# Kernel optimization log

Hardware: AMD Instinct MI355X
Metric: run time of the kernel (lower is better)

Reference implementation:

```python
import jax, jax.numpy as jnp
import numpy as np

B, S, D = 2, 2048, 2048
H = 16
HD = D // H  # 128
ROPE_THETA = 10000.0
NEG_INF = -1e9


def _rope_tables(seqlen, head_dim):
    inv = 1.0 / (ROPE_THETA ** (np.arange(0, head_dim, 2, dtype=np.float32) / head_dim))
    t = np.arange(seqlen, dtype=np.float32)
    freqs = np.outer(t, inv)  # (S, HD/2)
    return jnp.asarray(np.cos(freqs)), jnp.asarray(np.sin(freqs))


def _apply_rope(x, cos, sin):
    # x: (B, S, H, HD); cos/sin: (S, HD/2) -> complex multiply on (even, odd) pairs
    x = x.reshape(*x.shape[:-1], HD // 2, 2)
    x0, x1 = x[..., 0], x[..., 1]
    c = cos[None, :, None, :]
    s = sin[None, :, None, :]
    o0 = x0 * c - x1 * s
    o1 = x0 * s + x1 * c
    return jnp.stack([o0, o1], axis=-1).reshape(*x.shape[:-2], HD)


def setup_inputs() -> dict:
    key = jax.random.key(0)
    ks = jax.random.split(key, 6)
    std = 1.0 / np.sqrt(D)
    x = jax.random.normal(ks[0], (B, S, D), dtype=jnp.float32)
    wq = jax.random.normal(ks[1], (D, D), dtype=jnp.float32) * std
    wk = jax.random.normal(ks[2], (D, D), dtype=jnp.float32) * std
    wv = jax.random.normal(ks[3], (D, D), dtype=jnp.float32) * std
    wo = jax.random.normal(ks[4], (D, D), dtype=jnp.float32) * std
    cos, sin = _rope_tables(S, HD)
    # additive causal mask
    mask = jnp.where(jnp.tril(jnp.ones((S, S), dtype=bool)), 0.0, NEG_INF).astype(jnp.float32)
    return {"x": x, "wq": wq, "wk": wk, "wv": wv, "wo": wo, "cos": cos, "sin": sin, "mask": mask, "start_p": 0}


def reference(x, wq, wk, wv, wo, cos, sin, mask, start_p):
    bsz, seqlen, _ = x.shape
    xq = (x @ wq.T).reshape(bsz, seqlen, H, HD)
    xk = (x @ wk.T).reshape(bsz, seqlen, H, HD)
    xv = (x @ wv.T).reshape(bsz, seqlen, H, HD)
    c = cos[start_p:start_p + seqlen]
    s = sin[start_p:start_p + seqlen]
    xq = _apply_rope(xq, c, s)
    xk = _apply_rope(xk, c, s)
    # (B, H, S, HD)
    q = xq.transpose(0, 2, 1, 3)
    k = xk.transpose(0, 2, 1, 3)
    v = xv.transpose(0, 2, 1, 3)
    scores = jnp.einsum("bhqd,bhkd->bhqk", q, k) / np.sqrt(HD).astype(np.float32)
    scores = scores + mask[None, None, :, :]
    probs = jax.nn.softmax(scores.astype(jnp.float32), axis=-1).astype(q.dtype)
    out = jnp.einsum("bhqk,bhkd->bhqd", probs, v)
    out = out.transpose(0, 2, 1, 3).reshape(bsz, seqlen, H * HD)
    return out @ wo.T
```

## Files before the change

kernel.cpp:

```cpp
#include <hip/hip_runtime.h>
#include <cstdint>
#include <cstddef>

typedef unsigned short u16;
typedef unsigned int u32;
typedef __attribute__((ext_vector_type(8))) short short8;
typedef __attribute__((ext_vector_type(2))) unsigned int u32x2;
typedef __attribute__((ext_vector_type(8))) __bf16 bf16x8;
typedef __attribute__((ext_vector_type(4))) float f32x4;

#define BB 2
#define SS 2048
#define DD 2048
#define HH 16
#define HD 128

__device__ __forceinline__ u16 f2bf(float x) {
  u32 u = __float_as_uint(x);
  u32 r = (u + 0x7FFFu + ((u >> 16) & 1u)) >> 16;
  return (u16)r;
}
__device__ __forceinline__ float bf2f(u16 h) {
  return __uint_as_float(((u32)h) << 16);
}
__device__ __forceinline__ float exp2_hw(float x) {
  return __builtin_amdgcn_exp2f(x);
}
__device__ __forceinline__ u32 cvtpk_bf16(float lo, float hi) {
  u32 r;
  asm("v_cvt_pk_bf16_f32 %0, %1, %2" : "=v"(r) : "v"(lo), "v"(hi));
  return r;
}

__device__ __forceinline__ f32x4 mfma16x16x32(short8 a, short8 b, f32x4 c) {
  return __builtin_amdgcn_mfma_f32_16x16x32_bf16(
      __builtin_bit_cast(bf16x8, a), __builtin_bit_cast(bf16x8, b), c, 0, 0, 0);
}

__device__ __forceinline__ void gload_lds16(const void* g, void* l) {
  __builtin_amdgcn_global_load_lds(
      (const __attribute__((address_space(1))) void*)g,
      (__attribute__((address_space(3))) void*)l, 16, 0, 0);
}

__global__ void cast_all_kernel(const float* __restrict__ x,
                                const float* __restrict__ wq, const float* __restrict__ wk,
                                const float* __restrict__ wv, const float* __restrict__ wo,
                                u16* __restrict__ xb, u16* __restrict__ wb) {
  int g = blockIdx.x * blockDim.x + threadIdx.x;
  const float* s;
  u16* d;
  if (g < 1048576) {
    s = x + (size_t)g * 8;
    d = xb + (size_t)g * 8;
  } else {
    int wi = g - 1048576;
    int reg = wi >> 19;
    int off = wi & ((1 << 19) - 1);
    s = ((reg == 0) ? wq : (reg == 1) ? wk : (reg == 2) ? wv : wo) + (size_t)off * 8;
    d = wb + (size_t)wi * 8;
  }
  f32x4 a = *reinterpret_cast<const f32x4*>(s);
  f32x4 b = *reinterpret_cast<const f32x4*>(s + 4);
  short8 o;
  o[0] = (short)f2bf(a[0]); o[1] = (short)f2bf(a[1]);
  o[2] = (short)f2bf(a[2]); o[3] = (short)f2bf(a[3]);
  o[4] = (short)f2bf(b[0]); o[5] = (short)f2bf(b[1]);
  o[6] = (short)f2bf(b[2]); o[7] = (short)f2bf(b[3]);
  *reinterpret_cast<short8*>(d) = o;
}

template <int MODE>
__global__ __launch_bounds__(256) void gemm_nt(const u16* __restrict__ A,
                                               const u16* __restrict__ Bw,
                                               void* __restrict__ Cout,
                                               const float* __restrict__ cosT,
                                               const float* __restrict__ sinT) {
  constexpr int K = 2048, N = 2048;
  __shared__ u16 As[128 * 64];
  __shared__ u16 Bs[128 * 64];
  const int t = threadIdx.x;
  const int w = t >> 6, l = t & 63;
  const int bm = blockIdx.x, bn = blockIdx.y;
  const int wm = (w >> 1) * 64, wn = (w & 1) * 64;
  const int lr = l & 15, lg = l >> 4;
  f32x4 acc[4][4] = {};

  for (int kk = 0; kk < K; kk += 64) {
    __syncthreads();
#pragma unroll
    for (int i = 0; i < 4; ++i) {
      int cb = (i * 4 + w) * 64;
      int chunk = cb + l;
      int row = chunk >> 3, kc = chunk & 7;
      int lc = kc ^ (row & 7);
      gload_lds16(A + (size_t)(bm * 128 + row) * K + kk + lc * 8, (u16*)As + cb * 8);
      gload_lds16(Bw + (size_t)(bn * 128 + row) * K + kk + lc * 8, (u16*)Bs + cb * 8);
    }
    __syncthreads();
#pragma unroll
    for (int kh = 0; kh < 2; ++kh) {
      short8 af[4], bf[4];
#pragma unroll
      for (int mi = 0; mi < 4; ++mi) {
        int row = wm + mi * 16 + lr;
        int inner = (kh * 64 + lg * 16) ^ ((row & 7) << 4);
        af[mi] = *reinterpret_cast<const short8*>((const char*)As + row * 128 + inner);
      }
#pragma unroll
      for (int ni = 0; ni < 4; ++ni) {
        int row = wn + ni * 16 + lr;
        int inner = (kh * 64 + lg * 16) ^ ((row & 7) << 4);
        bf[ni] = *reinterpret_cast<const short8*>((const char*)Bs + row * 128 + inner);
      }
#pragma unroll
      for (int mi = 0; mi < 4; ++mi)
#pragma unroll
        for (int ni = 0; ni < 4; ++ni)
          acc[mi][ni] = mfma16x16x32(af[mi], bf[ni], acc[mi][ni]);
    }
  }
#pragma unroll
  for (int mi = 0; mi < 4; ++mi)
#pragma unroll
    for (int ni = 0; ni < 4; ++ni)
#pragma unroll
      for (int r = 0; r < 4; ++r) {
        int row = bm * 128 + wm + mi * 16 + lg * 4 + r;
        int col = bn * 128 + wn + ni * 16 + lr;
        float v = acc[mi][ni][r];
        if (MODE == 2) {
          float p = __shfl_xor(v, 1);
          int s = row & (SS - 1);
          int pi = (col & (HD - 1)) >> 1;
          float co = cosT[s * 64 + pi], sn = sinT[s * 64 + pi];
          v = (col & 1) ? (p * sn + v * co) : (v * co - p * sn);
        }
        if (MODE == 1)
          ((float*)Cout)[(size_t)row * N + col] = v;
        else
          ((u16*)Cout)[(size_t)row * N + col] = f2bf(v);
      }
}

__global__ __launch_bounds__(512, 2) void attn_kernel(const u16* __restrict__ XQ,
                                                      const u16* __restrict__ XK,
                                                      const u16* __restrict__ XV,
                                                      u16* __restrict__ AO) {
  __shared__ u16 Ks[2][64 * 128];
  __shared__ u16 Vs[2][128 * 64];
  __shared__ u16 Ps[8][16 * 64];
  const int ib = blockIdx.x, bh = blockIdx.y;
  const int b = bh >> 4, h = bh & 15;
  const int t = threadIdx.x, w = t >> 6, l = t & 63;
  const int wh = w >> 2, wl = w & 3;
  const int lr = l & 15, lg = l >> 4;
  const int qtA = 2 * ib + wh;
  const int qtB = 31 - 2 * ib - wh;
  const int qbA = qtA * 64 + wl * 16;
  const int qbB = qtB * 64 + wl * 16;
  const int nkv = 32 - 2 * ib;
  const size_t rowbase = (size_t)b * SS;

  const short one_bf = (short)0x3F80;
  const short8 onesf = {one_bf, one_bf, one_bf, one_bf, one_bf, one_bf, one_bf, one_bf};

  short8 qfA[4], qfB[4];
  {
    const u16* qpA = XQ + (rowbase + qbA + lr) * DD + h * HD + lg * 8;
    const u16* qpB = XQ + (rowbase + qbB + lr) * DD + h * HD + lg * 8;
#pragma unroll
    for (int ks = 0; ks < 4; ++ks) {
      qfA[ks] = *reinterpret_cast<const short8*>(qpA + ks * 32);
      qfB[ks] = *reinterpret_cast<const short8*>(qpB + ks * 32);
    }
  }

  f32x4 oA[8] = {}, oB[8] = {};
  f32x4 lsA = {}, lsB = {};
  float mrA = -1e30f, mrB = -1e30f;

  char* Pw = (char*)Ps[w];
  short8 vr[2];
  const int vk0 = (t >> 4) * 2;
  const int vd0 = (t & 15) * 8;

  auto issueK = [&](int kvt, int buf) {
#pragma unroll
    for (int i2 = 0; i2 < 2; ++i2) {
      int cb = (w * 2 + i2) * 64;
      int chunk = cb + l;
      int krow = chunk >> 4, kc = chunk & 15;
      int lc = kc ^ (krow & 7);
      gload_lds16(XK + (rowbase + kvt * 64 + krow) * DD + h * HD + lc * 8,
                  (u16*)Ks[buf] + cb * 8);
    }
  };
  auto loadV = [&](int kvt) {
    const u16* vp = XV + (rowbase + kvt * 64 + vk0) * DD + h * HD + vd0;
    vr[0] = *reinterpret_cast<const short8*>(vp);
    vr[1] = *reinterpret_cast<const short8*>(vp + DD);
  };
  auto writeV = [&](int buf) {
    char* base = (char*)Vs[buf];
#pragma unroll
    for (int ii = 0; ii < 8; ++ii) {
      int d = vd0 + ii;
      int off = d * 128 + ((vk0 * 2) ^ ((((d >> 3) & 7) ^ (d & 7)) << 4));
      u32 pk = (u32)(u16)vr[0][ii] | ((u32)(u16)vr[1][ii] << 16);
      *reinterpret_cast<u32*>(base + off) = pk;
    }
  };

  auto softmax_pv = [&](int kv, int cur, f32x4* sf, float& mr, f32x4& lsa, f32x4* o, int qbase) {
    const float scale2 = 0.12751743f;
    const bool diag = (kv == (qbase >> 6));
    const int kv0 = kv * 64;
    float pb[4][4];
#pragma unroll
    for (int kt = 0; kt < 4; ++kt)
#pragma unroll
      for (int r = 0; r < 4; ++r) {
        float s = sf[kt][r] * scale2;
        if (diag) {
          int kg = kv0 + kt * 16 + lg * 4 + r;
          int qg = qbase + lr;
          if (kg > qg) s = -1e30f;
        }
        pb[kt][r] = s;
      }
    float lm = pb[0][0];
#pragma unroll
    for (int kt = 0; kt < 4; ++kt)
#pragma unroll
      for (int r = 0; r < 4; ++r) lm = fmaxf(lm, pb[kt][r]);
    if (__any((int)(lm > mr + 11.54f))) {
      float m = lm;
      m = fmaxf(m, __shfl_xor(m, 16));
      m = fmaxf(m, __shfl_xor(m, 32));
      float mn = fmaxf(mr, m);
      float sc = exp2_hw(mr - mn);
      mr = mn;
#pragma unroll
      for (int r = 0; r < 4; ++r) {
        float scr = __shfl(sc, (l & 48) + lg * 4 + r);
        lsa[r] *= scr;
#pragma unroll
        for (int dt = 0; dt < 8; ++dt) o[dt][r] *= scr;
      }
    }
#pragma unroll
    for (int kt = 0; kt < 4; ++kt)
#pragma unroll
      for (int r = 0; r < 4; ++r)
        pb[kt][r] = exp2_hw(pb[kt][r] - mr);
    char* Pr = Pw + lr * 128;
    const int swz = (lr & 7) << 4;
#pragma unroll
    for (int kt = 0; kt < 4; ++kt) {
      u32x2 wv;
      wv[0] = cvtpk_bf16(pb[kt][0], pb[kt][1]);
      wv[1] = cvtpk_bf16(pb[kt][2], pb[kt][3]);
      *reinterpret_cast<u32x2*>(Pr + ((kt * 32 + lg * 8) ^ swz)) = wv;
    }
    short8 pa[2];
#pragma unroll
    for (int ks = 0; ks < 2; ++ks)
      pa[ks] = *reinterpret_cast<const short8*>(Pr + ((ks * 64 + lg * 16) ^ swz));
    lsa = mfma16x16x32(pa[0], onesf, lsa);
    lsa = mfma16x16x32(pa[1], onesf, lsa);
    const char* vbase = (const char*)Vs[cur];
#pragma unroll
    for (int dt = 0; dt < 8; ++dt)
#pragma unroll
      for (int ks = 0; ks < 2; ++ks) {
        int d = dt * 16 + lr;
        int off = d * 128 + ((ks * 64 + lg * 16) ^ ((((d >> 3) & 7) ^ (d & 7)) << 4));
        short8 vf = *reinterpret_cast<const short8*>(vbase + off);
        o[dt] = mfma16x16x32(pa[ks], vf, o[dt]);
      }
  };

  issueK(0, 0);
  loadV(0);

  for (int kv = 0; kv < nkv; ++kv) {
    const int cur = kv & 1;
    writeV(cur);
    __syncthreads();
    if (kv + 1 < nkv) { issueK(kv + 1, cur ^ 1); loadV(kv + 1); }

    const bool doB = (kv <= qtB);
    const bool doA = (kv <= qtA);
    if (doB) {
      f32x4 sB[4], sA[4];
#pragma unroll
      for (int kt = 0; kt < 4; ++kt) {
        sB[kt] = f32x4{0.f, 0.f, 0.f, 0.f};
        sA[kt] = f32x4{0.f, 0.f, 0.f, 0.f};
      }
#pragma unroll
      for (int kt = 0; kt < 4; ++kt) {
        short8 kf[4];
#pragma unroll
        for (int ks = 0; ks < 4; ++ks) {
          int krow = kt * 16 + lr;
          int inner = (ks * 64 + lg * 16) ^ ((krow & 7) << 4);
          kf[ks] = *reinterpret_cast<const short8*>((const char*)Ks[cur] + krow * 256 + inner);
        }
#pragma unroll
        for (int ks = 0; ks < 4; ++ks) sB[kt] = mfma16x16x32(kf[ks], qfB[ks], sB[kt]);
        if (doA) {
#pragma unroll
          for (int ks = 0; ks < 4; ++ks) sA[kt] = mfma16x16x32(kf[ks], qfA[ks], sA[kt]);
        }
      }
      softmax_pv(kv, cur, sB, mrB, lsB, oB, qbB);
      if (doA) softmax_pv(kv, cur, sA, mrA, lsA, oA, qbA);
    }
  }

#pragma unroll
  for (int r = 0; r < 4; ++r) {
    float invB = 1.0f / lsB[r];
    float invA = 1.0f / lsA[r];
    int qgB = qbB + lg * 4 + r;
    int qgA = qbA + lg * 4 + r;
    u16* opB = AO + (rowbase + qgB) * DD + h * HD + lr;
    u16* opA = AO + (rowbase + qgA) * DD + h * HD + lr;
#pragma unroll
    for (int dt = 0; dt < 8; ++dt) {
      opB[dt * 16] = f2bf(oB[dt][r] * invB);
      opA[dt * 16] = f2bf(oA[dt][r] * invA);
    }
  }
}

extern "C" void kernel_launch(void* const* d_in, const int* in_sizes, int n_in,
                              void* d_out, int out_size, void* d_ws, size_t ws_size,
                              hipStream_t stream) {
  const float* x = (const float*)d_in[0];
  const float* wq = (const float*)d_in[1];
  const float* wk = (const float*)d_in[2];
  const float* wv = (const float*)d_in[3];
  const float* wo = (const float*)d_in[4];
  const float* cosT = (const float*)d_in[5];
  const float* sinT = (const float*)d_in[6];

  char* ws = (char*)d_ws;
  u16* xb  = (u16*)(ws);
  u16* wqb = (u16*)(ws + 16777216);
  u16* wkb = (u16*)(ws + 25165824);
  u16* wvb = (u16*)(ws + 33554432);
  u16* wob = (u16*)(ws + 41943040);
  u16* XQ  = (u16*)(ws + 50331648);
  u16* XK  = (u16*)(ws + 67108864);
  u16* XV  = (u16*)(ws + 83886080);
  u16* AO  = (u16*)(ws + 100663296);

  cast_all_kernel<<<12288, 256, 0, stream>>>(x, wq, wk, wv, wo, xb, wqb);

  dim3 gg(32, 16);
  gemm_nt<2><<<gg, 256, 0, stream>>>(xb, wqb, XQ, cosT, sinT);
  gemm_nt<2><<<gg, 256, 0, stream>>>(xb, wkb, XK, cosT, sinT);
  gemm_nt<0><<<gg, 256, 0, stream>>>(xb, wvb, XV, nullptr, nullptr);

  attn_kernel<<<dim3(8, 32), 512, 0, stream>>>(XQ, XK, XV, AO);

  gemm_nt<1><<<gg, 256, 0, stream>>>(AO, wob, d_out, nullptr, nullptr);
}
```

Before: 287.5 us.

## Double-buffer GEMM LDS tiles and enlarge block tile to 256x128 with 8 waves

The projection GEMM now uses two LDS buffers, so global-to-LDS loads for the next k-tile are issued before computing the current one, with vmcnt waits in place of full syncs. The block tile grows to 256x128 with 512 threads (8 waves), halving the grid and reusing each B tile across more rows. This is meant to hide global load latency and cut B-tile traffic, at the cost of doubled LDS (96KB) and lower occupancy. It also depends on the vmcnt count matching the number of outstanding loads.

```diff
diff --git a/kernel.cpp b/kernel.cpp
--- a/kernel.cpp
+++ b/kernel.cpp
@@ -71,33 +71,56 @@
 }
 
 template <int MODE>
-__global__ __launch_bounds__(256) void gemm_nt(const u16* __restrict__ A,
+__global__ __launch_bounds__(512) void gemm_nt(const u16* __restrict__ A,
                                                const u16* __restrict__ Bw,
                                                void* __restrict__ Cout,
                                                const float* __restrict__ cosT,
                                                const float* __restrict__ sinT) {
   constexpr int K = 2048, N = 2048;
-  __shared__ u16 As[128 * 64];
-  __shared__ u16 Bs[128 * 64];
+  __shared__ u16 As[2][256 * 64];
+  __shared__ u16 Bs[2][128 * 64];
   const int t = threadIdx.x;
   const int w = t >> 6, l = t & 63;
   const int bm = blockIdx.x, bn = blockIdx.y;
-  const int wm = (w >> 1) * 64, wn = (w & 1) * 64;
+  const int wm = (w >> 1) * 64;
+  const int wn = (w & 1) * 64;
   const int lr = l & 15, lg = l >> 4;
   f32x4 acc[4][4] = {};
 
-  for (int kk = 0; kk < K; kk += 64) {
-    __syncthreads();
-#pragma unroll
-    for (int i = 0; i < 4; ++i) {
-      int cb = (i * 4 + w) * 64;
+  auto ISSUE = [&](int kt, int buf) {
+    const int kk = kt * 64;
+#pragma unroll
+    for (int i = 0; i < 6; ++i) {
+      int cb = (i * 8 + w) * 64;
       int chunk = cb + l;
-      int row = chunk >> 3, kc = chunk & 7;
-      int lc = kc ^ (row & 7);
-      gload_lds16(A + (size_t)(bm * 128 + row) * K + kk + lc * 8, (u16*)As + cb * 8);
-      gload_lds16(Bw + (size_t)(bn * 128 + row) * K + kk + lc * 8, (u16*)Bs + cb * 8);
-    }
-    __syncthreads();
+      if (chunk < 2048) {
+        int row = chunk >> 3, kc = chunk & 7;
+        int lc = kc ^ (row & 7);
+        gload_lds16(A + (size_t)(bm * 256 + row) * K + kk + lc * 8,
+                    (u16*)As[buf] + chunk * 8);
+      } else {
+        int c2 = chunk - 2048;
+        int row = c2 >> 3, kc = c2 & 7;
+        int lc = kc ^ (row & 7);
+        gload_lds16(Bw + (size_t)(bn * 128 + row) * K + kk + lc * 8,
+                    (u16*)Bs[buf] + c2 * 8);
+      }
+    }
+  };
+
+  ISSUE(0, 0);
+
+  for (int kt = 0; kt < 32; ++kt) {
+    const int cur = kt & 1;
+    __builtin_amdgcn_s_barrier();
+    if (kt + 1 < 32) {
+      ISSUE(kt + 1, cur ^ 1);
+      asm volatile("s_waitcnt vmcnt(6)" ::: "memory");
+    } else {
+      asm volatile("s_waitcnt vmcnt(0)" ::: "memory");
+    }
+    __builtin_amdgcn_s_barrier();
+
 #pragma unroll
     for (int kh = 0; kh < 2; ++kh) {
       short8 af[4], bf[4];
@@ -105,13 +128,13 @@
       for (int mi = 0; mi < 4; ++mi) {
         int row = wm + mi * 16 + lr;
         int inner = (kh * 64 + lg * 16) ^ ((row & 7) << 4);
-        af[mi] = *reinterpret_cast<const short8*>((const char*)As + row * 128 + inner);
+        af[mi] = *reinterpret_cast<const short8*>((const char*)As[cur] + row * 128 + inner);
       }
 #pragma unroll
       for (int ni = 0; ni < 4; ++ni) {
         int row = wn + ni * 16 + lr;
         int inner = (kh * 64 + lg * 16) ^ ((row & 7) << 4);
-        bf[ni] = *reinterpret_cast<const short8*>((const char*)Bs + row * 128 + inner);
+        bf[ni] = *reinterpret_cast<const short8*>((const char*)Bs[cur] + row * 128 + inner);
       }
 #pragma unroll
       for (int mi = 0; mi < 4; ++mi)
@@ -120,13 +143,14 @@
           acc[mi][ni] = mfma16x16x32(af[mi], bf[ni], acc[mi][ni]);
     }
   }
+
 #pragma unroll
   for (int mi = 0; mi < 4; ++mi)
 #pragma unroll
     for (int ni = 0; ni < 4; ++ni)
 #pragma unroll
       for (int r = 0; r < 4; ++r) {
-        int row = bm * 128 + wm + mi * 16 + lg * 4 + r;
+        int row = bm * 256 + wm + mi * 16 + lg * 4 + r;
         int col = bn * 128 + wn + ni * 16 + lr;
         float v = acc[mi][ni][r];
         if (MODE == 2) {
@@ -360,12 +384,12 @@
 
   cast_all_kernel<<<12288, 256, 0, stream>>>(x, wq, wk, wv, wo, xb, wqb);
 
-  dim3 gg(32, 16);
-  gemm_nt<2><<<gg, 256, 0, stream>>>(xb, wqb, XQ, cosT, sinT);
-  gemm_nt<2><<<gg, 256, 0, stream>>>(xb, wkb, XK, cosT, sinT);
-  gemm_nt<0><<<gg, 256, 0, stream>>>(xb, wvb, XV, nullptr, nullptr);
+  dim3 gg(16, 16);
+  gemm_nt<2><<<gg, 512, 0, stream>>>(xb, wqb, XQ, cosT, sinT);
+  gemm_nt<2><<<gg, 512, 0, stream>>>(xb, wkb, XK, cosT, sinT);
+  gemm_nt<0><<<gg, 512, 0, stream>>>(xb, wvb, XV, nullptr, nullptr);
 
   attn_kernel<<<dim3(8, 32), 512, 0, stream>>>(XQ, XK, XV, AO);
 
-  gemm_nt<1><<<gg, 256, 0, stream>>>(AO, wob, d_out, nullptr, nullptr);
-}
+  gemm_nt<1><<<gg, 512, 0, stream>>>(AO, wob, d_out, nullptr, nullptr);
+}
```

New measurement: 307.1 us. 6.8% more time.
